# Performance work log

Measured on AMD Instinct MI355X. Metric: run time of the kernel, lower is better.

Reference implementation:

```python
import jax, jax.numpy as jnp
import numpy as np

N_HEAD = 32
N_KV_HEAD = 8
ROPE_THETA = 500000.0


def rotate_half(x):
    d = x.shape[-1] // 2
    return jnp.concatenate((-x[..., d:], x[..., :d]), axis=-1)


def setup_inputs() -> dict:
    key = jax.random.key(0)
    ks = jax.random.split(key, 5)
    C = 2048
    B, T = 2, 2048
    s = 1.0 / np.sqrt(C)
    return {
        "x": jax.random.normal(ks[0], (B, T, C), dtype=jnp.float32),
        "Wq": jax.random.normal(ks[1], (C, C), dtype=jnp.float32) * s,
        "Wk": jax.random.normal(ks[2], (C, 512), dtype=jnp.float32) * s,
        "Wv": jax.random.normal(ks[3], (C, 512), dtype=jnp.float32) * s,
        "Wo": jax.random.normal(ks[4], (C, C), dtype=jnp.float32) * s,
    }


def reference(x, Wq, Wk, Wv, Wo):
    B, T, C = x.shape
    H, KV = N_HEAD, N_KV_HEAD
    D = C // H
    n_rep = H // KV

    q = (x @ Wq).reshape(B, T, H, D).transpose(0, 2, 1, 3)   # [B,H,T,D]
    k = (x @ Wk).reshape(B, T, KV, D).transpose(0, 2, 1, 3)  # [B,KV,T,D]
    v = (x @ Wv).reshape(B, T, KV, D).transpose(0, 2, 1, 3)  # [B,KV,T,D]

    # RoPE: cos/sin of shape [1,1,T,D], broadcast over batch and heads
    inv_freq = 1.0 / (ROPE_THETA ** (jnp.arange(0, D, 2, dtype=jnp.float32) / D))
    freqs = jnp.arange(T, dtype=jnp.float32)[:, None] * inv_freq[None, :]  # [T,D/2]
    emb = jnp.concatenate((freqs, freqs), axis=-1)  # [T,D]
    cos = jnp.cos(emb)[None, None].astype(x.dtype)
    sin = jnp.sin(emb)[None, None].astype(x.dtype)

    q = q * cos + rotate_half(q) * sin
    k = k * cos + rotate_half(k) * sin

    # repeat_kv (GQA expansion): [B,KV,T,D] -> [B,H,T,D]
    k = jnp.repeat(k, n_rep, axis=1)
    v = jnp.repeat(v, n_rep, axis=1)

    scale = 1.0 / jnp.sqrt(jnp.asarray(D, dtype=x.dtype))
    scores = jnp.einsum("bhqd,bhkd->bhqk", q, k) * scale  # [B,H,T,T]
    causal = jnp.tril(jnp.ones((T, T), dtype=bool))
    scores = jnp.where(causal[None, None], scores, jnp.finfo(scores.dtype).min)
    attn = jax.nn.softmax(scores, axis=-1)
    y = jnp.einsum("bhqk,bhkd->bhqd", attn, v)  # [B,H,T,D]
    y = y.transpose(0, 2, 1, 3).reshape(B, T, C)
    return y @ Wo
```

## Files before the change

kernel.cpp:

```cpp
#include <hip/hip_runtime.h>

using u16 = unsigned short;
using u32 = unsigned int;

typedef __attribute__((ext_vector_type(8))) __bf16 bf16x8;
typedef __attribute__((ext_vector_type(4))) float f32x4;
typedef __attribute__((ext_vector_type(16))) float f32x16;

#define DEVI __device__ __forceinline__

DEVI float bf2f(u16 u) {
  union { u32 i; float f; } v; v.i = ((u32)u) << 16; return v.f;
}
DEVI u16 f2bf(float f) {
  union { float f; u32 u; } v; v.f = f;
  u32 u = v.u;
  u32 r = (u + 0x7fffu + ((u >> 16) & 1u)) >> 16;
  return (u16)r;
}
DEVI u32 pkbf(float a, float b) {
  union { __bf16 h[2]; u32 u; } t;
  t.h[0] = (__bf16)a; t.h[1] = (__bf16)b;
  return t.u;
}

DEVI void gload16(const u16* g, u16* l) {
  __builtin_amdgcn_global_load_lds(
      (const __attribute__((address_space(1))) void*)g,
      (__attribute__((address_space(3))) void*)l, 16, 0, 0);
}

__global__ __launch_bounds__(256) void cvt_bf16_f32(const float* __restrict__ in,
                                                    u16* __restrict__ out, int n8) {
  int i = blockIdx.x * 256 + threadIdx.x;
  if (i >= n8) return;
  const float4* fin = (const float4*)in;
  float4 a = fin[i * 2], b = fin[i * 2 + 1];
  u16 o[8] = {f2bf(a.x), f2bf(a.y), f2bf(a.z), f2bf(a.w),
              f2bf(b.x), f2bf(b.y), f2bf(b.z), f2bf(b.w)};
  ((uint4*)out)[i] = *(const uint4*)o;
}

__global__ __launch_bounds__(256) void transpose_cvt(const float* __restrict__ in,
                                                     u16* __restrict__ out,
                                                     int R, int Cc) {
  __shared__ u16 tile[32][33];
  int c0 = blockIdx.x * 32, r0 = blockIdx.y * 32;
  int x  = threadIdx.x & 31;
  int y0 = threadIdx.x >> 5;
  for (int yy = y0; yy < 32; yy += 8)
    tile[yy][x] = f2bf(in[(size_t)(r0 + yy) * Cc + c0 + x]);
  __syncthreads();
  for (int yy = y0; yy < 32; yy += 8)
    out[(size_t)(c0 + yy) * R + r0 + x] = tile[x][yy];
}

__global__ __launch_bounds__(256) void transpose_sl(const u16* __restrict__ in, int ldin,
                                                    u16* __restrict__ out,
                                                    int R, int Cc) {
  __shared__ u16 tile[32][33];
  int c0 = blockIdx.x * 32, r0 = blockIdx.y * 32;
  int x  = threadIdx.x & 31;
  int y0 = threadIdx.x >> 5;
  for (int yy = y0; yy < 32; yy += 8)
    tile[yy][x] = in[(size_t)(r0 + yy) * ldin + c0 + x];
  __syncthreads();
  for (int yy = y0; yy < 32; yy += 8)
    out[(size_t)(c0 + yy) * R + r0 + x] = tile[x][yy];
}

__global__ __launch_bounds__(256) void rope_k(u16* __restrict__ X, int ld, int width, int total) {
  int idx = blockIdx.x * 256 + threadIdx.x;
  if (idx >= total) return;
  int ppr  = width >> 1;
  int row  = idx / ppr;
  int rem  = idx - row * ppr;
  int head = rem >> 5;
  int d    = rem & 31;
  int t    = row & 2047;
  float inv = exp2f(-(float)d * 0.59161152f);
  float ang = (float)t * inv;
  float s, c;
  sincosf(ang, &s, &c);
  size_t base = (size_t)row * ld + head * 64 + d;
  float x0 = bf2f(X[base]);
  float x1 = bf2f(X[base + 32]);
  X[base]      = f2bf(x0 * c - x1 * s);
  X[base + 32] = f2bf(x1 * c + x0 * s);
}

DEVI void cstore(u16* C, size_t idx, float v)   { C[idx] = f2bf(v); }
DEVI void cstore(float* C, size_t idx, float v) { C[idx] = v; }

template <typename TO>
__global__ __launch_bounds__(256) void gemm128(const u16* __restrict__ A,
                                               const u16* __restrict__ Bt,
                                               TO* __restrict__ C,
                                               int M, int N, int K) {
  __shared__ u16 As[128 * 32];
  __shared__ u16 Bs[128 * 32];
  int tid = threadIdx.x, wid = tid >> 6, lane = tid & 63;
  int quad = lane >> 4, l15 = lane & 15;
  int m0 = blockIdx.y * 128, n0 = blockIdx.x * 128;
  int wm = (wid >> 1) * 64, wn = (wid & 1) * 64;

  int r0s = wid * 16 + (lane >> 2);
  int r1s = 64 + wid * 16 + (lane >> 2);
  int cblk = lane & 3;
  int cs0 = (cblk ^ ((r0s >> 1) & 3)) * 8;
  int cs1 = (cblk ^ ((r1s >> 1) & 3)) * 8;
  u16* lA0 = As + wid * 512 + lane * 8;
  u16* lA1 = As + (4 + wid) * 512 + lane * 8;
  u16* lB0 = Bs + wid * 512 + lane * 8;
  u16* lB1 = Bs + (4 + wid) * 512 + lane * 8;
  const u16* gA0 = A + (size_t)(m0 + r0s) * K + cs0;
  const u16* gA1 = A + (size_t)(m0 + r1s) * K + cs1;
  const u16* gB0 = Bt + (size_t)(n0 + r0s) * K + cs0;
  const u16* gB1 = Bt + (size_t)(n0 + r1s) * K + cs1;

  f32x4 acc[4][4];
  for (int i = 0; i < 4; i++)
    for (int j = 0; j < 4; j++) acc[i][j] = f32x4{0.f, 0.f, 0.f, 0.f};

  for (int k0 = 0; k0 < K; k0 += 32) {
    __syncthreads();
    gload16(gA0 + k0, lA0);
    gload16(gA1 + k0, lA1);
    gload16(gB0 + k0, lB0);
    gload16(gB1 + k0, lB1);
    __builtin_amdgcn_s_waitcnt(0x0F70);
    __syncthreads();
    bf16x8 af[4], bf_[4];
    for (int mi = 0; mi < 4; mi++) {
      int row = wm + mi * 16 + l15;
      af[mi] = *(const bf16x8*)(As + row * 32 + ((quad ^ ((row >> 1) & 3)) * 8));
    }
    for (int ni = 0; ni < 4; ni++) {
      int row = wn + ni * 16 + l15;
      bf_[ni] = *(const bf16x8*)(Bs + row * 32 + ((quad ^ ((row >> 1) & 3)) * 8));
    }
    for (int mi = 0; mi < 4; mi++)
      for (int ni = 0; ni < 4; ni++)
        acc[mi][ni] = __builtin_amdgcn_mfma_f32_16x16x32_bf16(af[mi], bf_[ni], acc[mi][ni], 0, 0, 0);
  }
  for (int mi = 0; mi < 4; mi++)
    for (int ni = 0; ni < 4; ni++)
      for (int r = 0; r < 4; r++) {
        int row = m0 + wm + mi * 16 + quad * 4 + r;
        int col = n0 + wn + ni * 16 + l15;
        cstore(C, (size_t)row * N + col, acc[mi][ni][r]);
      }
}

__global__ __launch_bounds__(256) void attn64(const u16* __restrict__ QKV,
                                              const u16* __restrict__ Vt,
                                              u16* __restrict__ Y) {
  __shared__ u16 Ks[2 * 64 * 64];
  __shared__ u16 Vst[2 * 64 * 64];

  int tid = threadIdx.x, wid = tid >> 6, lane = tid & 63;
  int l31 = lane & 31, hi = lane >> 5;
  int bh = blockIdx.y, b = bh >> 5, h = bh & 31, kvh = h >> 2;
  int p = blockIdx.x;

  const float sc_log2e = 0.18033688f;

  int kr  = wid * 8 + (lane >> 3);
  int kgn = lane & 7;
  const u16* gK0 = QKV + (size_t)(b * 2048 + kr) * 3072 + 2048 + kvh * 64
                 + ((kgn ^ (kr & 7)) * 8);
  u16* lK0 = Ks + wid * 512 + lane * 8;

  int vr = tid >> 3, vg = tid & 7;
  const u16* gV0 = Vt + (size_t)(kvh * 64 + vr) * 4096 + b * 2048 + vg * 8;
  u16* lV0 = Vst + vr * 64 + ((vg ^ (vr & 7)) * 8);

  for (int pass = 0; pass < 2; pass++) {
    int j   = pass ? (15 - p) : p;
    int q0w = j * 128 + wid * 32;
    int qg  = q0w + l31;

    bf16x8 qf[4];
    {
      const u16* qp = QKV + (size_t)(b * 2048 + qg) * 3072 + h * 64 + hi * 8;
#pragma unroll
      for (int dh = 0; dh < 4; dh++) qf[dh] = *(const bf16x8*)(qp + dh * 16);
    }

    f32x16 o0, o1;
#pragma unroll
    for (int i = 0; i < 16; i++) { o0[i] = 0.f; o1[i] = 0.f; }
    float zsum = 0.f;

    int nkt = 2 * (j + 1);

    {
      uint4 va = *(const uint4*)(gV0);
      uint4 vb = *(const uint4*)(gV0 + 32 * 4096);
      gload16(gK0, lK0);
      gload16(gK0 + 32 * 3072, lK0 + 2048);
      __builtin_amdgcn_s_waitcnt(0x0F70);
      *(uint4*)(lV0)        = va;
      *(uint4*)(lV0 + 2048) = vb;
    }
    __syncthreads();

    int cur = 0;
    for (int kt = 0; kt < nkt; kt++) {
      int kbase = kt * 64;
      int nxt = cur ^ 1;
      bool more = (kt + 1 < nkt);
      uint4 va, vb;
      if (more) {
        size_t ko = (size_t)(kbase + 64);
        va = *(const uint4*)(gV0 + ko);
        vb = *(const uint4*)(gV0 + 32 * 4096 + ko);
        gload16(gK0 + ko * 3072, lK0 + nxt * 4096);
        gload16(gK0 + ko * 3072 + 32 * 3072, lK0 + nxt * 4096 + 2048);
      }

      const u16* Kb = Ks + cur * 4096;
      const u16* Vb = Vst + cur * 4096;
#pragma unroll
      for (int sub = 0; sub < 2; sub++) {
        int kb = kbase + sub * 32;
        if (kb > q0w) break;

        f32x16 s;
#pragma unroll
        for (int i = 0; i < 16; i++) s[i] = 0.f;
#pragma unroll
        for (int dh = 0; dh < 4; dh++) {
          int g = (dh * 2 + hi) ^ (l31 & 7);
          bf16x8 kf = *(const bf16x8*)(Kb + (sub * 32 + l31) * 64 + g * 8);
          s = __builtin_amdgcn_mfma_f32_32x32x16_bf16(kf, qf[dh], s, 0, 0, 0);
        }

        float pb[16];
        if (kb < q0w) {
#pragma unroll
          for (int r = 0; r < 16; r++) {
            float pv = exp2f(s[r] * sc_log2e);
            zsum += pv;
            pb[r] = pv;
          }
        } else {
#pragma unroll
          for (int r = 0; r < 16; r++) {
            int key = kb + (r & 3) + 8 * (r >> 2) + 4 * hi;
            float pv = (key <= qg) ? exp2f(s[r] * sc_log2e) : 0.f;
            zsum += pv;
            pb[r] = pv;
          }
        }

#pragma unroll
        for (int kk = 0; kk < 2; kk++) {
          const float* pp = pb + kk * 8;
          u32 a01 = pkbf(pp[0], pp[1]);
          u32 a23 = pkbf(pp[2], pp[3]);
          u32 a45 = pkbf(pp[4], pp[5]);
          u32 a67 = pkbf(pp[6], pp[7]);
          asm volatile("v_permlane32_swap_b32 %0, %1" : "+v"(a01), "+v"(a45));
          asm volatile("v_permlane32_swap_b32 %0, %1" : "+v"(a23), "+v"(a67));
          union { u32 w[4]; bf16x8 v; } pf;
          pf.w[0] = a01; pf.w[1] = a23; pf.w[2] = a45; pf.w[3] = a67;
          int kgr = sub * 4 + kk * 2 + hi;
          const u16* vp = Vb + l31 * 64 + ((kgr ^ (l31 & 7)) * 8);
          bf16x8 v0 = *(const bf16x8*)(vp);
          bf16x8 v1 = *(const bf16x8*)(vp + 2048);
          o0 = __builtin_amdgcn_mfma_f32_32x32x16_bf16(pf.v, v0, o0, 0, 0, 0);
          o1 = __builtin_amdgcn_mfma_f32_32x32x16_bf16(pf.v, v1, o1, 0, 0, 0);
        }
      }

      if (more) {
        __builtin_amdgcn_s_waitcnt(0x0F70);
        *(uint4*)(lV0 + nxt * 4096)        = va;
        *(uint4*)(lV0 + nxt * 4096 + 2048) = vb;
      }
      __syncthreads();
      cur = nxt;
    }

    float zf = zsum + __shfl_xor(zsum, 32);

#pragma unroll
    for (int r = 0; r < 16; r++) {
      int qr = (r & 3) + 8 * (r >> 2) + 4 * hi;
      float zr = __shfl(zf, qr, 64);
      float inv = 1.f / zr;
      size_t row = (size_t)(b * 2048 + q0w + qr);
      Y[row * 2048 + h * 64 + l31]      = f2bf(o0[r] * inv);
      Y[row * 2048 + h * 64 + 32 + l31] = f2bf(o1[r] * inv);
    }
  }
}

extern "C" void kernel_launch(void* const* d_in, const int* in_sizes, int n_in,
                              void* d_out, int out_size, void* d_ws, size_t ws_size,
                              hipStream_t stream) {
  const float* x  = (const float*)d_in[0];
  const float* Wq = (const float*)d_in[1];
  const float* Wk = (const float*)d_in[2];
  const float* Wv = (const float*)d_in[3];
  const float* Wo = (const float*)d_in[4];
  float* outp = (float*)d_out;

  u16* xb    = (u16*)d_ws;
  u16* WqkvT = xb + 8388608;
  u16* QKV   = WqkvT + 6291456;
  u16* Vt    = QKV + 12582912;
  u16* Yb    = xb;
  u16* WoT   = WqkvT;

  cvt_bf16_f32<<<4096, 256, 0, stream>>>(x, xb, 1048576);

  transpose_cvt<<<dim3(64, 64), 256, 0, stream>>>(Wq, WqkvT, 2048, 2048);
  transpose_cvt<<<dim3(16, 64), 256, 0, stream>>>(Wk, WqkvT + (size_t)2048 * 2048, 2048, 512);
  transpose_cvt<<<dim3(16, 64), 256, 0, stream>>>(Wv, WqkvT + (size_t)2560 * 2048, 2048, 512);

  gemm128<u16><<<dim3(24, 32), 256, 0, stream>>>(xb, WqkvT, QKV, 4096, 3072, 2048);

  rope_k<<<(4096 * 1024) / 256, 256, 0, stream>>>(QKV, 3072, 2048, 4096 * 1024);
  rope_k<<<(4096 * 256) / 256, 256, 0, stream>>>(QKV + 2048, 3072, 512, 4096 * 256);

  transpose_sl<<<dim3(16, 128), 256, 0, stream>>>(QKV + 2560, 3072, Vt, 4096, 512);

  attn64<<<dim3(8, 64), 256, 0, stream>>>(QKV, Vt, Yb);

  transpose_cvt<<<dim3(64, 64), 256, 0, stream>>>(Wo, WoT, 2048, 2048);
  gemm128<float><<<dim3(16, 32), 256, 0, stream>>>(Yb, WoT, outp, 4096, 2048, 2048);
}
```

Before: 351.4 us.

## Double-buffer GEMM LDS tiles, vectorize transposes and RoPE, fold softmax scale into Q

The GEMM now keeps two LDS stages and issues the next K-tile's global-to-LDS loads before computing the current one, which removes one barrier per iteration and overlaps load latency with MFMA work. The transpose kernels move to 64x64 tiles with 16-byte vector loads and stores. RoPE is vectorized over 8 elements per thread, uses fast __sincosf, and steps the frequency by repeated multiplication. The softmax scale times log2e is folded into Q during RoPE, so attention skips one multiply per score. The fast sincos and the multiplicative frequency recurrence may cost some accuracy, and LDS use in the GEMM doubles.

```diff
diff --git a/kernel.cpp b/kernel.cpp
--- a/kernel.cpp
+++ b/kernel.cpp
@@ -41,52 +41,93 @@
   ((uint4*)out)[i] = *(const uint4*)o;
 }
 
-__global__ __launch_bounds__(256) void transpose_cvt(const float* __restrict__ in,
-                                                     u16* __restrict__ out,
-                                                     int R, int Cc) {
-  __shared__ u16 tile[32][33];
-  int c0 = blockIdx.x * 32, r0 = blockIdx.y * 32;
-  int x  = threadIdx.x & 31;
-  int y0 = threadIdx.x >> 5;
-  for (int yy = y0; yy < 32; yy += 8)
-    tile[yy][x] = f2bf(in[(size_t)(r0 + yy) * Cc + c0 + x]);
+__global__ __launch_bounds__(256) void transpose_cvt64(const float* __restrict__ in,
+                                                       u16* __restrict__ out,
+                                                       int R, int Cc) {
+  __shared__ u16 tile[64][72];
+  int c0 = blockIdx.x * 64, r0 = blockIdx.y * 64;
+  int t = threadIdx.x;
+  {
+    int row = t >> 2, part = t & 3;
+    const float* src = in + (size_t)(r0 + row) * Cc + c0 + part * 16;
+    float4 f0 = ((const float4*)src)[0];
+    float4 f1 = ((const float4*)src)[1];
+    float4 f2 = ((const float4*)src)[2];
+    float4 f3 = ((const float4*)src)[3];
+    u16 v[16] = {f2bf(f0.x), f2bf(f0.y), f2bf(f0.z), f2bf(f0.w),
+                 f2bf(f1.x), f2bf(f1.y), f2bf(f1.z), f2bf(f1.w),
+                 f2bf(f2.x), f2bf(f2.y), f2bf(f2.z), f2bf(f2.w),
+                 f2bf(f3.x), f2bf(f3.y), f2bf(f3.z), f2bf(f3.w)};
+    *(uint4*)&tile[row][part * 16]     = ((const uint4*)v)[0];
+    *(uint4*)&tile[row][part * 16 + 8] = ((const uint4*)v)[1];
+  }
   __syncthreads();
-  for (int yy = y0; yy < 32; yy += 8)
-    out[(size_t)(c0 + yy) * R + r0 + x] = tile[x][yy];
-}
-
-__global__ __launch_bounds__(256) void transpose_sl(const u16* __restrict__ in, int ldin,
-                                                    u16* __restrict__ out,
-                                                    int R, int Cc) {
-  __shared__ u16 tile[32][33];
-  int c0 = blockIdx.x * 32, r0 = blockIdx.y * 32;
-  int x  = threadIdx.x & 31;
-  int y0 = threadIdx.x >> 5;
-  for (int yy = y0; yy < 32; yy += 8)
-    tile[yy][x] = in[(size_t)(r0 + yy) * ldin + c0 + x];
+  {
+    int c = t & 63, rq = t >> 6;
+    u16 v[16];
+#pragma unroll
+    for (int i = 0; i < 16; i++) v[i] = tile[rq * 16 + i][c];
+    u16* dst = out + (size_t)(c0 + c) * R + r0 + rq * 16;
+    ((uint4*)dst)[0] = ((const uint4*)v)[0];
+    ((uint4*)dst)[1] = ((const uint4*)v)[1];
+  }
+}
+
+__global__ __launch_bounds__(256) void transpose_sl64(const u16* __restrict__ in, int ldin,
+                                                      u16* __restrict__ out,
+                                                      int R, int Cc) {
+  __shared__ u16 tile[64][72];
+  int c0 = blockIdx.x * 64, r0 = blockIdx.y * 64;
+  int t = threadIdx.x;
+  {
+    int row = t >> 2, part = t & 3;
+    const u16* src = in + (size_t)(r0 + row) * ldin + c0 + part * 16;
+    uint4 a = ((const uint4*)src)[0];
+    uint4 b = ((const uint4*)src)[1];
+    *(uint4*)&tile[row][part * 16]     = a;
+    *(uint4*)&tile[row][part * 16 + 8] = b;
+  }
   __syncthreads();
-  for (int yy = y0; yy < 32; yy += 8)
-    out[(size_t)(c0 + yy) * R + r0 + x] = tile[x][yy];
-}
-
-__global__ __launch_bounds__(256) void rope_k(u16* __restrict__ X, int ld, int width, int total) {
+  {
+    int c = t & 63, rq = t >> 6;
+    u16 v[16];
+#pragma unroll
+    for (int i = 0; i < 16; i++) v[i] = tile[rq * 16 + i][c];
+    u16* dst = out + (size_t)(c0 + c) * R + r0 + rq * 16;
+    ((uint4*)dst)[0] = ((const uint4*)v)[0];
+    ((uint4*)dst)[1] = ((const uint4*)v)[1];
+  }
+}
+
+__global__ __launch_bounds__(256) void rope_v(u16* __restrict__ X, int ld, int h4shift,
+                                              float scale, int total) {
   int idx = blockIdx.x * 256 + threadIdx.x;
   if (idx >= total) return;
-  int ppr  = width >> 1;
-  int row  = idx / ppr;
-  int rem  = idx - row * ppr;
-  int head = rem >> 5;
-  int d    = rem & 31;
-  int t    = row & 2047;
-  float inv = exp2f(-(float)d * 0.59161152f);
-  float ang = (float)t * inv;
-  float s, c;
-  sincosf(ang, &s, &c);
-  size_t base = (size_t)row * ld + head * 64 + d;
-  float x0 = bf2f(X[base]);
-  float x1 = bf2f(X[base + 32]);
-  X[base]      = f2bf(x0 * c - x1 * s);
-  X[base + 32] = f2bf(x1 * c + x0 * s);
+  int hq   = idx & ((1 << h4shift) - 1);
+  int row  = idx >> h4shift;
+  int head = hq >> 2;
+  int d0   = (hq & 3) * 8;
+  int tpos = row & 2047;
+  size_t base = (size_t)row * ld + head * 64 + d0;
+  uint4 lo = *(const uint4*)(X + base);
+  uint4 hi = *(const uint4*)(X + base + 32);
+  const u16* lp = (const u16*)&lo;
+  const u16* hp = (const u16*)&hi;
+  float ang = (float)tpos * exp2f(-(float)d0 * 0.59161152f);
+  u16 o0[8], o1[8];
+#pragma unroll
+  for (int i = 0; i < 8; i++) {
+    float s, c;
+    __sincosf(ang, &s, &c);
+    s *= scale; c *= scale;
+    float x0 = bf2f(lp[i]);
+    float x1 = bf2f(hp[i]);
+    o0[i] = f2bf(x0 * c - x1 * s);
+    o1[i] = f2bf(x1 * c + x0 * s);
+    ang *= 0.6636011f;
+  }
+  *(uint4*)(X + base)      = *(const uint4*)o0;
+  *(uint4*)(X + base + 32) = *(const uint4*)o1;
 }
 
 DEVI void cstore(u16* C, size_t idx, float v)   { C[idx] = f2bf(v); }
@@ -97,8 +138,8 @@
                                                const u16* __restrict__ Bt,
                                                TO* __restrict__ C,
                                                int M, int N, int K) {
-  __shared__ u16 As[128 * 32];
-  __shared__ u16 Bs[128 * 32];
+  __shared__ u16 As[2 * 128 * 32];
+  __shared__ u16 Bs[2 * 128 * 32];
   int tid = threadIdx.x, wid = tid >> 6, lane = tid & 63;
   int quad = lane >> 4, l15 = lane & 15;
   int m0 = blockIdx.y * 128, n0 = blockIdx.x * 128;
@@ -122,26 +163,39 @@
   for (int i = 0; i < 4; i++)
     for (int j = 0; j < 4; j++) acc[i][j] = f32x4{0.f, 0.f, 0.f, 0.f};
 
+  gload16(gA0, lA0);
+  gload16(gA1, lA1);
+  gload16(gB0, lB0);
+  gload16(gB1, lB1);
+  __builtin_amdgcn_s_waitcnt(0x0F70);
+  __syncthreads();
+
+  int cur = 0;
   for (int k0 = 0; k0 < K; k0 += 32) {
-    __syncthreads();
-    gload16(gA0 + k0, lA0);
-    gload16(gA1 + k0, lA1);
-    gload16(gB0 + k0, lB0);
-    gload16(gB1 + k0, lB1);
-    __builtin_amdgcn_s_waitcnt(0x0F70);
-    __syncthreads();
+    int nb = cur ^ 1;
+    if (k0 + 32 < K) {
+      gload16(gA0 + k0 + 32, lA0 + nb * 4096);
+      gload16(gA1 + k0 + 32, lA1 + nb * 4096);
+      gload16(gB0 + k0 + 32, lB0 + nb * 4096);
+      gload16(gB1 + k0 + 32, lB1 + nb * 4096);
+    }
+    const u16* Ab = As + cur * 4096;
+    const u16* Bb = Bs + cur * 4096;
     bf16x8 af[4], bf_[4];
     for (int mi = 0; mi < 4; mi++) {
       int row = wm + mi * 16 + l15;
-      af[mi] = *(const bf16x8*)(As + row * 32 + ((quad ^ ((row >> 1) & 3)) * 8));
+      af[mi] = *(const bf16x8*)(Ab + row * 32 + ((quad ^ ((row >> 1) & 3)) * 8));
     }
     for (int ni = 0; ni < 4; ni++) {
       int row = wn + ni * 16 + l15;
-      bf_[ni] = *(const bf16x8*)(Bs + row * 32 + ((quad ^ ((row >> 1) & 3)) * 8));
+      bf_[ni] = *(const bf16x8*)(Bb + row * 32 + ((quad ^ ((row >> 1) & 3)) * 8));
     }
     for (int mi = 0; mi < 4; mi++)
       for (int ni = 0; ni < 4; ni++)
         acc[mi][ni] = __builtin_amdgcn_mfma_f32_16x16x32_bf16(af[mi], bf_[ni], acc[mi][ni], 0, 0, 0);
+    __builtin_amdgcn_s_waitcnt(0x0F70);
+    __syncthreads();
+    cur = nb;
   }
   for (int mi = 0; mi < 4; mi++)
     for (int ni = 0; ni < 4; ni++)
@@ -162,8 +216,6 @@
   int l31 = lane & 31, hi = lane >> 5;
   int bh = blockIdx.y, b = bh >> 5, h = bh & 31, kvh = h >> 2;
   int p = blockIdx.x;
-
-  const float sc_log2e = 0.18033688f;
 
   int kr  = wid * 8 + (lane >> 3);
   int kgn = lane & 7;
@@ -240,7 +292,7 @@
         if (kb < q0w) {
 #pragma unroll
           for (int r = 0; r < 16; r++) {
-            float pv = exp2f(s[r] * sc_log2e);
+            float pv = exp2f(s[r]);
             zsum += pv;
             pb[r] = pv;
           }
@@ -248,7 +300,7 @@
 #pragma unroll
           for (int r = 0; r < 16; r++) {
             int key = kb + (r & 3) + 8 * (r >> 2) + 4 * hi;
-            float pv = (key <= qg) ? exp2f(s[r] * sc_log2e) : 0.f;
+            float pv = (key <= qg) ? exp2f(s[r]) : 0.f;
             zsum += pv;
             pb[r] = pv;
           }
@@ -316,19 +368,19 @@
 
   cvt_bf16_f32<<<4096, 256, 0, stream>>>(x, xb, 1048576);
 
-  transpose_cvt<<<dim3(64, 64), 256, 0, stream>>>(Wq, WqkvT, 2048, 2048);
-  transpose_cvt<<<dim3(16, 64), 256, 0, stream>>>(Wk, WqkvT + (size_t)2048 * 2048, 2048, 512);
-  transpose_cvt<<<dim3(16, 64), 256, 0, stream>>>(Wv, WqkvT + (size_t)2560 * 2048, 2048, 512);
+  transpose_cvt64<<<dim3(32, 32), 256, 0, stream>>>(Wq, WqkvT, 2048, 2048);
+  transpose_cvt64<<<dim3(8, 32), 256, 0, stream>>>(Wk, WqkvT + (size_t)2048 * 2048, 2048, 512);
+  transpose_cvt64<<<dim3(8, 32), 256, 0, stream>>>(Wv, WqkvT + (size_t)2560 * 2048, 2048, 512);
 
   gemm128<u16><<<dim3(24, 32), 256, 0, stream>>>(xb, WqkvT, QKV, 4096, 3072, 2048);
 
-  rope_k<<<(4096 * 1024) / 256, 256, 0, stream>>>(QKV, 3072, 2048, 4096 * 1024);
-  rope_k<<<(4096 * 256) / 256, 256, 0, stream>>>(QKV + 2048, 3072, 512, 4096 * 256);
-
-  transpose_sl<<<dim3(16, 128), 256, 0, stream>>>(QKV + 2560, 3072, Vt, 4096, 512);
+  rope_v<<<2048, 256, 0, stream>>>(QKV, 3072, 7, 0.18033688f, 4096 * 128);
+  rope_v<<<512, 256, 0, stream>>>(QKV + 2048, 3072, 5, 1.0f, 4096 * 32);
+
+  transpose_sl64<<<dim3(8, 64), 256, 0, stream>>>(QKV + 2560, 3072, Vt, 4096, 512);
 
   attn64<<<dim3(8, 64), 256, 0, stream>>>(QKV, Vt, Yb);
 
-  transpose_cvt<<<dim3(64, 64), 256, 0, stream>>>(Wo, WoT, 2048, 2048);
+  transpose_cvt64<<<dim3(32, 32), 256, 0, stream>>>(Wo, WoT, 2048, 2048);
   gemm128<float><<<dim3(16, 32), 256, 0, stream>>>(Yb, WoT, outp, 4096, 2048, 2048);
 }
```

Result: faster. 329.6 us (-6.2%).
